# Kernel optimization log

Measured on AMD Instinct MI355X. Metric: run time of the kernel, lower is better.

## Reference

```python
import jax, jax.numpy as jnp
import numpy as np

MAX_REL = 128  # max_relative_position


def setup_inputs() -> dict:
    key = jax.random.key(0)
    k1, k2, k3, k4 = jax.random.split(key, 4)
    B, H, S, D = 2, 8, 2048, 64
    q = jax.random.normal(k1, (B, H, S, D), dtype=jnp.float32)
    k = jax.random.normal(k2, (B, H, S, D), dtype=jnp.float32)
    v = jax.random.normal(k3, (B, H, S, D), dtype=jnp.float32)
    rel_table = jax.random.normal(k4, (2 * MAX_REL + 1, D), dtype=jnp.float32)
    return {"q": q, "k": k, "v": v, "rel_table": rel_table}


def reference(q, k, v, rel_table):
    B, H, S, D = q.shape
    scale = jnp.sqrt(jnp.asarray(D, q.dtype))
    # content scores: [B,H,S,S]
    qk_scores = jnp.einsum('bhqd,bhkd->bhqk', q, k)
    # relative position index matrix [S,S] clamped to [-MAX_REL, MAX_REL]
    pos = jnp.arange(S)
    rel_idx = jnp.clip(pos[None, :] - pos[:, None], -MAX_REL, MAX_REL) + MAX_REL
    rel_emb = rel_table[rel_idx]  # [S,S,D]
    # relative scores: per-query dot with rel embedding row -> [B,H,S,S]
    rel_scores = jnp.einsum('bhqd,qkd->bhqk', q, rel_emb)
    scores = (qk_scores + rel_scores) / scale
    attn = jax.nn.softmax(scores, axis=-1)
    # output: [B,H,S,D]
    return jnp.einsum('bhqk,bhkd->bhqd', attn, v)
```

## Files before the change

kernel.cpp:

```cpp
#include <hip/hip_runtime.h>

typedef _Float16 half8 __attribute__((ext_vector_type(8)));
typedef _Float16 half4 __attribute__((ext_vector_type(4)));
typedef float f32x4 __attribute__((ext_vector_type(4)));

#define S_LEN 2048
#define HDIM 64
#define QBLK 64
#define KVBLK 64
#define NT (S_LEN / KVBLK)
#define QRS 258
#define NBH 16
#define L2E 1.44269504f
#define TSTR 72

__device__ __forceinline__ void load_lds16(const void* g, void* l) {
    __builtin_amdgcn_global_load_lds(
        (const __attribute__((address_space(1))) unsigned int*)g,
        (__attribute__((address_space(3))) unsigned int*)l, 16, 0, 0);
}

__global__ __launch_bounds__(256)
void convert_kv_kernel(const float* __restrict__ Kg, const float* __restrict__ Vg,
                       _Float16* __restrict__ Kh, _Float16* __restrict__ Vp)
{
    __shared__ _Float16 tile[KVBLK * TSTR];
    const int bid = blockIdx.x;
    const int tid = threadIdx.x;
    if (bid < 1024) {
        const int id = bid * 256 + tid;
        const int r  = id >> 3;
        const int d0 = (id & 7) * 8;
        const float* src = Kg + (size_t)r * HDIM + d0;
        f32x4 f0 = *(const f32x4*)(src);
        f32x4 f1 = *(const f32x4*)(src + 4);
        half8 h;
#pragma unroll
        for (int j = 0; j < 4; ++j) { h[j] = (_Float16)f0[j]; h[j+4] = (_Float16)f1[j]; }
        const int bh = r >> 11, kvg = r & 2047;
        const int t = kvg >> 6, kv = kvg & 63;
        const size_t blk = (size_t)(bh * NT + t) * 8192;
        const int off = (kv * 128 + d0 * 2) ^ ((kv & 7) << 4);
        *(half8*)((char*)Kh + blk + off) = h;
    } else {
        const int bt = bid - 1024;
        const int bh = bt >> 5, t = bt & 31;
        {
            const int kv = tid >> 2;
            const int d0 = (tid & 3) * 16;
            const float* src = Vg + ((size_t)bh * S_LEN + t * KVBLK + kv) * HDIM + d0;
            f32x4 f0 = *(const f32x4*)(src);
            f32x4 f1 = *(const f32x4*)(src + 4);
            f32x4 f2 = *(const f32x4*)(src + 8);
            f32x4 f3 = *(const f32x4*)(src + 12);
            half8 h0, h1;
#pragma unroll
            for (int j = 0; j < 4; ++j) {
                h0[j] = (_Float16)f0[j]; h0[j+4] = (_Float16)f1[j];
                h1[j] = (_Float16)f2[j]; h1[j+4] = (_Float16)f3[j];
            }
            *(half8*)&tile[kv * TSTR + d0]     = h0;
            *(half8*)&tile[kv * TSTR + d0 + 8] = h1;
        }
        __syncthreads();
        {
            const int dp = tid >> 2;
            const int u0 = (tid & 3) * 2;
            char* base = (char*)Vp + (size_t)bt * 8192;
            const int swz = (dp & 7) << 4;
#pragma unroll
            for (int ui = 0; ui < 2; ++ui) {
                const int u  = u0 + ui;
                const int kc = u >> 2, g = u & 3;
                half8 ch;
#pragma unroll
                for (int r = 0; r < 4; ++r) {
                    ch[r]     = tile[(32*kc + 4*g + r)      * TSTR + dp];
                    ch[4 + r] = tile[(32*kc + 16 + 4*g + r) * TSTR + dp];
                }
                *(half8*)(base + ((dp * 128 + u * 16) ^ swz)) = ch;
            }
        }
    }
}

__global__ __launch_bounds__(256, 2)
void relattn_v3(const float* __restrict__ Qg, const float* __restrict__ RELg,
                const _Float16* __restrict__ Kh, const _Float16* __restrict__ Vp,
                float* __restrict__ Og)
{
    __shared__ __attribute__((aligned(16))) _Float16 Kbuf[2][4096];
    __shared__ __attribute__((aligned(16))) _Float16 Vbuf[2][4096];
    __shared__ __attribute__((aligned(16))) _Float16 Qrel[QBLK * QRS];

    const int tid  = threadIdx.x;
    const int wave = tid >> 6;
    const int lane = tid & 63;
    const int c = lane & 15;
    const int g = lane >> 4;

    const int wk = ((blockIdx.x & 7) << 6) + (blockIdx.x >> 3);
    const int bh = wk >> 5;
    const int q0 = (wk & 31) * QBLK;

    const size_t hoff = (size_t)bh * S_LEN * HDIM;

    const int qg_ = q0 + wave * 16 + c;
    half8 aq[2];
#pragma unroll
    for (int kc = 0; kc < 2; ++kc) {
        const float* src = Qg + hoff + (size_t)qg_ * HDIM + kc * 32 + g * 8;
        f32x4 f0 = *(const f32x4*)(src);
        f32x4 f1 = *(const f32x4*)(src + 4);
        half8 h;
#pragma unroll
        for (int j = 0; j < 4; ++j) {
            h[j]     = (_Float16)(f0[j] * 0.125f);
            h[j + 4] = (_Float16)(f1[j] * 0.125f);
        }
        aq[kc] = h;
    }

#pragma unroll 1
    for (int t = 0; t < 17; ++t) {
        f32x4 acc = {0.f, 0.f, 0.f, 0.f};
        int r = t * 16 + c;
        if (r > 256) r = 256;
#pragma unroll
        for (int kc = 0; kc < 2; ++kc) {
            const float* src = RELg + (size_t)r * HDIM + kc * 32 + g * 8;
            f32x4 f0 = *(const f32x4*)(src);
            f32x4 f1 = *(const f32x4*)(src + 4);
            half8 b;
#pragma unroll
            for (int j = 0; j < 4; ++j) { b[j] = (_Float16)f0[j]; b[j+4] = (_Float16)f1[j]; }
            acc = __builtin_amdgcn_mfma_f32_16x16x32_f16(aq[kc], b, acc, 0, 0, 0);
        }
        const int col = t * 16 + c;
        if (col <= 256) {
#pragma unroll
            for (int reg = 0; reg < 4; ++reg)
                Qrel[(wave * 16 + 4 * g + reg) * QRS + col] = (_Float16)acc[reg];
        }
    }
    asm volatile("s_waitcnt lgkmcnt(0)" ::: "memory");
    const _Float16* qr = &Qrel[(wave * 16 + c) * QRS];
    const float bias_lo = (float)qr[0];
    const float bias_hi = (float)qr[256];

    const int swz  = (c & 7) << 4;
    const int off0 = (g * 16) ^ swz;
    const int off1 = (64 + g * 16) ^ swz;
    const char* kp0 = (const char*)Kbuf + c * 128 + off0;
    const char* kp1 = (const char*)Kbuf + c * 128 + off1;
    const char* vp0 = (const char*)Vbuf + c * 128 + off0;
    const char* vp1 = (const char*)Vbuf + c * 128 + off1;

    half8 ones;
#pragma unroll
    for (int j = 0; j < 8; ++j) ones[j] = (_Float16)1.0f;

    float m = -1e30f;
    f32x4 l_acc = {0.f, 0.f, 0.f, 0.f};
    f32x4 oacc[4];
#pragma unroll
    for (int i = 0; i < 4; ++i) oacc[i] = (f32x4){0.f, 0.f, 0.f, 0.f};

    const char* kbase = (const char*)Kh + (size_t)(bh * NT) * 8192;
    const char* vbase = (const char*)Vp + (size_t)(bh * NT) * 8192;
    const int goff = wave * 2048 + lane * 16;
    const int loff = wave * 2048;

#define ISSUE(tt, bb) do {                                              \
        const char* kt = kbase + (size_t)(tt) * 8192 + goff;            \
        const char* vt = vbase + (size_t)(tt) * 8192 + goff;            \
        char* kl = (char*)Kbuf + (bb) * 8192 + loff;                    \
        char* vl = (char*)Vbuf + (bb) * 8192 + loff;                    \
        load_lds16(kt,        kl);                                      \
        load_lds16(kt + 1024, kl + 1024);                               \
        load_lds16(vt,        vl);                                      \
        load_lds16(vt + 1024, vl + 1024);                               \
    } while (0)

#define BODY(t, b) do {                                                              \
        if ((t) + 1 < NT) {                                                          \
            ISSUE((t) + 1, (b) ^ 1);                                                 \
            asm volatile("s_waitcnt vmcnt(4)" ::: "memory");                         \
        } else {                                                                     \
            asm volatile("s_waitcnt vmcnt(0)" ::: "memory");                         \
        }                                                                            \
        __builtin_amdgcn_s_barrier();                                                \
        const int k0 = (t) * KVBLK;                                                  \
        f32x4 sacc[4];                                                               \
        _Pragma("unroll")                                                            \
        for (int n = 0; n < 4; ++n) sacc[n] = (f32x4){0.f,0.f,0.f,0.f};              \
        __builtin_amdgcn_s_setprio(1);                                               \
        _Pragma("unroll")                                                            \
        for (int n = 0; n < 4; ++n) {                                                \
            half8 ak0 = *(const half8*)(kp0 + (b) * 8192 + n * 2048);                \
            sacc[n] = __builtin_amdgcn_mfma_f32_16x16x32_f16(ak0, aq[0], sacc[n], 0, 0, 0); \
        }                                                                            \
        _Pragma("unroll")                                                            \
        for (int n = 0; n < 4; ++n) {                                                \
            half8 ak1 = *(const half8*)(kp1 + (b) * 8192 + n * 2048);                \
            sacc[n] = __builtin_amdgcn_mfma_f32_16x16x32_f16(ak1, aq[1], sacc[n], 0, 0, 0); \
        }                                                                            \
        __builtin_amdgcn_s_setprio(0);                                               \
        const bool band = (k0 + 192 > q0) && (k0 < q0 + 192);                        \
        float fold; float mtb;                                                       \
        if (!band) {                                                                 \
            const float bc = (k0 < q0) ? bias_lo : bias_hi;                          \
            float mt = sacc[0][0];                                                   \
            _Pragma("unroll")                                                        \
            for (int n = 0; n < 4; ++n)                                              \
                _Pragma("unroll")                                                    \
                for (int r = 0; r < 4; ++r) mt = fmaxf(mt, sacc[n][r]);              \
            mt = fmaxf(mt, __shfl_xor(mt, 16, 64));                                  \
            mt = fmaxf(mt, __shfl_xor(mt, 32, 64));                                  \
            mtb = mt + bc;                                                           \
            if (!__all(mtb <= m + 8.f)) {                                            \
                const float mnew = fmaxf(m, mtb);                                    \
                const float al = __builtin_amdgcn_exp2f((m - mnew) * L2E);           \
                m = mnew;                                                            \
                _Pragma("unroll")                                                    \
                for (int r = 0; r < 4; ++r) {                                        \
                    const float ar = __shfl(al, 20 * g + r, 64);                     \
                    l_acc[r] *= ar;                                                  \
                    _Pragma("unroll")                                                \
                    for (int dn = 0; dn < 4; ++dn) oacc[dn][r] *= ar;                \
                }                                                                    \
            }                                                                        \
            fold = (bc - m) * L2E;                                                   \
        } else {                                                                     \
            const int base_d = k0 + 4 * g - qg_ + 128;                               \
            float mt = -1e30f;                                                       \
            _Pragma("unroll")                                                        \
            for (int n = 0; n < 4; ++n) {                                            \
                _Pragma("unroll")                                                    \
                for (int r = 0; r < 4; ++r) {                                        \
                    int idx = base_d + 16 * n + r;                                   \
                    idx = idx < 0 ? 0 : (idx > 256 ? 256 : idx);                     \
                    sacc[n][r] += (float)qr[idx];                                    \
                    mt = fmaxf(mt, sacc[n][r]);                                      \
                }                                                                    \
            }                                                                        \
            mt = fmaxf(mt, __shfl_xor(mt, 16, 64));                                  \
            mt = fmaxf(mt, __shfl_xor(mt, 32, 64));                                  \
            mtb = mt;                                                                \
            if (!__all(mtb <= m + 8.f)) {                                            \
                const float mnew = fmaxf(m, mtb);                                    \
                const float al = __builtin_amdgcn_exp2f((m - mnew) * L2E);           \
                m = mnew;                                                            \
                _Pragma("unroll")                                                    \
                for (int r = 0; r < 4; ++r) {                                        \
                    const float ar = __shfl(al, 20 * g + r, 64);                     \
                    l_acc[r] *= ar;                                                  \
                    _Pragma("unroll")                                                \
                    for (int dn = 0; dn < 4; ++dn) oacc[dn][r] *= ar;                \
                }                                                                    \
            }                                                                        \
            fold = -m * L2E;                                                         \
        }                                                                            \
        half4 p4[4];                                                                 \
        _Pragma("unroll")                                                            \
        for (int n = 0; n < 4; ++n) {                                                \
            _Pragma("unroll")                                                        \
            for (int r = 0; r < 4; ++r) {                                            \
                const float pv = __builtin_amdgcn_exp2f(fmaf(sacc[n][r], L2E, fold));\
                p4[n][r] = (_Float16)pv;                                             \
            }                                                                        \
        }                                                                            \
        half8 ap0, ap1;                                                              \
        _Pragma("unroll")                                                            \
        for (int r = 0; r < 4; ++r) {                                                \
            ap0[r] = p4[0][r]; ap0[4 + r] = p4[1][r];                                \
            ap1[r] = p4[2][r]; ap1[4 + r] = p4[3][r];                                \
        }                                                                            \
        __builtin_amdgcn_s_setprio(1);                                               \
        l_acc = __builtin_amdgcn_mfma_f32_16x16x32_f16(ap0, ones, l_acc, 0, 0, 0);   \
        l_acc = __builtin_amdgcn_mfma_f32_16x16x32_f16(ap1, ones, l_acc, 0, 0, 0);   \
        _Pragma("unroll")                                                            \
        for (int dn = 0; dn < 4; ++dn) {                                             \
            half8 bv0 = *(const half8*)(vp0 + (b) * 8192 + dn * 2048);               \
            oacc[dn] = __builtin_amdgcn_mfma_f32_16x16x32_f16(ap0, bv0, oacc[dn], 0, 0, 0); \
        }                                                                            \
        _Pragma("unroll")                                                            \
        for (int dn = 0; dn < 4; ++dn) {                                             \
            half8 bv1 = *(const half8*)(vp1 + (b) * 8192 + dn * 2048);               \
            oacc[dn] = __builtin_amdgcn_mfma_f32_16x16x32_f16(ap1, bv1, oacc[dn], 0, 0, 0); \
        }                                                                            \
        __builtin_amdgcn_s_setprio(0);                                               \
        __builtin_amdgcn_s_barrier();                                                \
    } while (0)

    ISSUE(0, 0);
#pragma unroll 1
    for (int tt = 0; tt < NT; tt += 2) {
        BODY(tt, 0);
        BODY(tt + 1, 1);
    }
#undef BODY
#undef ISSUE

#pragma unroll
    for (int r = 0; r < 4; ++r) {
        const float inv = 1.0f / l_acc[r];
        float* dst = Og + hoff + (size_t)(q0 + wave * 16 + 4 * g + r) * HDIM + c;
#pragma unroll
        for (int dn = 0; dn < 4; ++dn)
            dst[16 * dn] = oacc[dn][r] * inv;
    }
}

__global__ __launch_bounds__(256, 2)
void relattn_v1(const float* __restrict__ Qg, const float* __restrict__ Kg,
                const float* __restrict__ Vg, const float* __restrict__ RELg,
                float* __restrict__ Og)
{
    __shared__ _Float16 Klds[KVBLK * HDIM];
    __shared__ _Float16 Vt[HDIM * KVBLK];
    __shared__ _Float16 Plds[4][16 * KVBLK];
    __shared__ _Float16 Qrel[QBLK * QRS];

    const int tid  = threadIdx.x;
    const int wave = tid >> 6;
    const int lane = tid & 63;
    const int c = lane & 15;
    const int g = lane >> 4;

    const int bid = blockIdx.x;
    const int bh  = bid >> 5;
    const int q0  = (bid & 31) * QBLK;

    const size_t hoff = (size_t)bh * S_LEN * HDIM;
    const float* Qh = Qg + hoff;
    const float* Kh = Kg + hoff;
    const float* Vh = Vg + hoff;

    const int qrow_frag = q0 + wave * 16 + c;
    half8 aq[2];
#pragma unroll
    for (int kc = 0; kc < 2; ++kc) {
        const float* src = Qh + (size_t)qrow_frag * HDIM + kc * 32 + g * 8;
        f32x4 f0 = *(const f32x4*)(src);
        f32x4 f1 = *(const f32x4*)(src + 4);
        half8 h;
#pragma unroll
        for (int j = 0; j < 4; ++j) {
            h[j]     = (_Float16)(f0[j] * 0.125f);
            h[j + 4] = (_Float16)(f1[j] * 0.125f);
        }
        aq[kc] = h;
    }

#pragma unroll 1
    for (int t = 0; t < 17; ++t) {
        f32x4 acc = {0.f, 0.f, 0.f, 0.f};
        int r = t * 16 + c;
        if (r > 256) r = 256;
#pragma unroll
        for (int kc = 0; kc < 2; ++kc) {
            const float* src = RELg + (size_t)r * HDIM + kc * 32 + g * 8;
            f32x4 f0 = *(const f32x4*)(src);
            f32x4 f1 = *(const f32x4*)(src + 4);
            half8 b;
#pragma unroll
            for (int j = 0; j < 4; ++j) { b[j] = (_Float16)f0[j]; b[j+4] = (_Float16)f1[j]; }
            acc = __builtin_amdgcn_mfma_f32_16x16x32_f16(aq[kc], b, acc, 0, 0, 0);
        }
        const int col = t * 16 + c;
        if (col <= 256) {
#pragma unroll
            for (int reg = 0; reg < 4; ++reg)
                Qrel[(wave * 16 + 4 * g + reg) * QRS + col] = (_Float16)acc[reg];
        }
    }

    float mrow[4], lrow[4];
    f32x4 oacc[4];
#pragma unroll
    for (int i = 0; i < 4; ++i) {
        mrow[i] = -1e30f; lrow[i] = 0.f;
        oacc[i] = (f32x4){0.f, 0.f, 0.f, 0.f};
    }

    for (int k0 = 0; k0 < S_LEN; k0 += KVBLK) {
        __syncthreads();
        {
            const int r  = tid >> 2;
            const int dq = (tid & 3) << 4;
            const float* src = Kh + (size_t)(k0 + r) * HDIM + dq;
            f32x4 f0 = *(const f32x4*)(src);
            f32x4 f1 = *(const f32x4*)(src + 4);
            f32x4 f2 = *(const f32x4*)(src + 8);
            f32x4 f3 = *(const f32x4*)(src + 12);
            half8 h0, h1;
#pragma unroll
            for (int j = 0; j < 4; ++j) {
                h0[j] = (_Float16)f0[j]; h0[j+4] = (_Float16)f1[j];
                h1[j] = (_Float16)f2[j]; h1[j+4] = (_Float16)f3[j];
            }
            const int swz = (r & 7) << 4;
            char* base = (char*)Klds;
            *(half8*)(base + ((r * 128 + dq * 2) ^ swz))      = h0;
            *(half8*)(base + ((r * 128 + dq * 2 + 16) ^ swz)) = h1;
        }
        {
            const int kv = tid & 63;
            const int dbase = (tid >> 6) << 4;
            const float* src = Vh + (size_t)(k0 + kv) * HDIM + dbase;
            f32x4 f0 = *(const f32x4*)(src);
            f32x4 f1 = *(const f32x4*)(src + 4);
            f32x4 f2 = *(const f32x4*)(src + 8);
            f32x4 f3 = *(const f32x4*)(src + 12);
            float vals[16];
#pragma unroll
            for (int j = 0; j < 4; ++j) {
                vals[j] = f0[j]; vals[4+j] = f1[j]; vals[8+j] = f2[j]; vals[12+j] = f3[j];
            }
            char* base = (char*)Vt;
#pragma unroll
            for (int i = 0; i < 16; ++i) {
                const int d = dbase + i;
                const int off = (d * 128 + kv * 2) ^ ((d & 7) << 4);
                *(_Float16*)(base + off) = (_Float16)vals[i];
            }
        }
        __syncthreads();

        f32x4 sacc[4];
#pragma unroll
        for (int n = 0; n < 4; ++n) sacc[n] = (f32x4){0.f,0.f,0.f,0.f};
#pragma unroll
        for (int kc = 0; kc < 2; ++kc) {
#pragma unroll
            for (int n = 0; n < 4; ++n) {
                const int off = (((16*n + c) * 128) + kc * 64 + g * 16) ^ ((c & 7) << 4);
                half8 bk = *(const half8*)((const char*)Klds + off);
                sacc[n] = __builtin_amdgcn_mfma_f32_16x16x32_f16(aq[kc], bk, sacc[n], 0, 0, 0);
            }
        }

        float sval[4][4];
        const int myq0 = q0 + wave * 16 + 4 * g;
#pragma unroll
        for (int n = 0; n < 4; ++n) {
            const int kpos = k0 + 16 * n + c;
#pragma unroll
            for (int reg = 0; reg < 4; ++reg) {
                int rel = kpos - (myq0 + reg);
                rel = rel < -128 ? -128 : (rel > 128 ? 128 : rel);
                const float bias = (float)Qrel[(wave*16 + 4*g + reg) * QRS + (rel + 128)];
                sval[n][reg] = sacc[n][reg] + bias;
            }
        }

        float mt[4];
#pragma unroll
        for (int reg = 0; reg < 4; ++reg) {
            float mp = fmaxf(fmaxf(sval[0][reg], sval[1][reg]),
                             fmaxf(sval[2][reg], sval[3][reg]));
#pragma unroll
            for (int msk = 1; msk < 16; msk <<= 1)
                mp = fmaxf(mp, __shfl_xor(mp, msk, 64));
            mt[reg] = mp;
        }

        float alpha[4], psum[4];
#pragma unroll
        for (int reg = 0; reg < 4; ++reg) {
            const float mn = fmaxf(mrow[reg], mt[reg]);
            alpha[reg] = __expf(mrow[reg] - mn);
            mrow[reg] = mn;
            psum[reg] = 0.f;
        }

        char* pbase = (char*)&Plds[wave][0];
#pragma unroll
        for (int n = 0; n < 4; ++n) {
#pragma unroll
            for (int reg = 0; reg < 4; ++reg) {
                const float pv = __expf(sval[n][reg] - mrow[reg]);
                psum[reg] += pv;
                const int row = 4 * g + reg;
                const int off = (row * 128 + (16 * n + c) * 2) ^ ((row & 7) << 4);
                *(_Float16*)(pbase + off) = (_Float16)pv;
            }
        }

#pragma unroll
        for (int reg = 0; reg < 4; ++reg) {
            float ps = psum[reg];
#pragma unroll
            for (int msk = 1; msk < 16; msk <<= 1)
                ps += __shfl_xor(ps, msk, 64);
            lrow[reg] = lrow[reg] * alpha[reg] + ps;
#pragma unroll
            for (int dn = 0; dn < 4; ++dn) oacc[dn][reg] *= alpha[reg];
        }

        asm volatile("s_waitcnt lgkmcnt(0)" ::: "memory");

        half8 ap[2];
#pragma unroll
        for (int kc = 0; kc < 2; ++kc) {
            const int off = (c * 128 + kc * 64 + g * 16) ^ ((c & 7) << 4);
            ap[kc] = *(const half8*)(pbase + off);
        }
#pragma unroll
        for (int kc = 0; kc < 2; ++kc) {
#pragma unroll
            for (int dn = 0; dn < 4; ++dn) {
                const int drow = 16 * dn + c;
                const int off = (drow * 128 + kc * 64 + g * 16) ^ ((c & 7) << 4);
                half8 bv = *(const half8*)((const char*)Vt + off);
                oacc[dn] = __builtin_amdgcn_mfma_f32_16x16x32_f16(ap[kc], bv, oacc[dn], 0, 0, 0);
            }
        }
    }

#pragma unroll
    for (int reg = 0; reg < 4; ++reg) {
        const float inv = 1.0f / lrow[reg];
        const int row = q0 + wave * 16 + 4 * g + reg;
        float* dst = Og + hoff + (size_t)row * HDIM + c;
#pragma unroll
        for (int dn = 0; dn < 4; ++dn)
            dst[16 * dn] = oacc[dn][reg] * inv;
    }
}

extern "C" void kernel_launch(void* const* d_in, const int* in_sizes, int n_in,
                              void* d_out, int out_size, void* d_ws, size_t ws_size,
                              hipStream_t stream) {
    const float* q   = (const float*)d_in[0];
    const float* k   = (const float*)d_in[1];
    const float* v   = (const float*)d_in[2];
    const float* rel = (const float*)d_in[3];
    float* out = (float*)d_out;
    (void)in_sizes; (void)n_in; (void)out_size;

    const size_t kv_bytes = (size_t)NBH * S_LEN * HDIM * sizeof(_Float16);
    if (ws_size >= 2 * kv_bytes) {
        _Float16* KhB = (_Float16*)d_ws;
        _Float16* VpB = (_Float16*)((char*)d_ws + kv_bytes);
        convert_kv_kernel<<<dim3(1536), 256, 0, stream>>>(k, v, KhB, VpB);
        relattn_v3<<<dim3(NBH * (S_LEN / QBLK)), 256, 0, stream>>>(q, rel, KhB, VpB, out);
    } else {
        relattn_v1<<<dim3(NBH * (S_LEN / QBLK)), 256, 0, stream>>>(q, k, v, rel, out);
    }
}
```

Baseline: 63.49 us.

## Split KV range in two per query block with partial-softmax combine kernel

Doubles the grid by splitting each query block's KV sweep into two halves. Each half writes fp16 partial outputs plus per-row max and sum, and a new combine kernel merges them. V tiles are now read straight from global memory into registers with prefetch instead of being staged in LDS, which lowers LDS use so occupancy can rise to 3 blocks per CU. The costs are an extra kernel launch, round trips of the partials through global memory, fp16 rounding of the unnormalised partial outputs, and higher register pressure.

```diff
diff --git a/kernel.cpp b/kernel.cpp
--- a/kernel.cpp
+++ b/kernel.cpp
@@ -9,6 +9,7 @@
 #define QBLK 64
 #define KVBLK 64
 #define NT (S_LEN / KVBLK)
+#define NHALF 16
 #define QRS 258
 #define NBH 16
 #define L2E 1.44269504f
@@ -67,30 +68,29 @@
             const int dp = tid >> 2;
             const int u0 = (tid & 3) * 2;
             char* base = (char*)Vp + (size_t)bt * 8192;
-            const int swz = (dp & 7) << 4;
 #pragma unroll
             for (int ui = 0; ui < 2; ++ui) {
                 const int u  = u0 + ui;
-                const int kc = u >> 2, g = u & 3;
+                const int kc = u >> 2, gg = u & 3;
                 half8 ch;
 #pragma unroll
                 for (int r = 0; r < 4; ++r) {
-                    ch[r]     = tile[(32*kc + 4*g + r)      * TSTR + dp];
-                    ch[4 + r] = tile[(32*kc + 16 + 4*g + r) * TSTR + dp];
+                    ch[r]     = tile[(32*kc + 4*gg + r)      * TSTR + dp];
+                    ch[4 + r] = tile[(32*kc + 16 + 4*gg + r) * TSTR + dp];
                 }
-                *(half8*)(base + ((dp * 128 + u * 16) ^ swz)) = ch;
+                *(half8*)(base + dp * 128 + u * 16) = ch;
             }
         }
     }
 }
 
-__global__ __launch_bounds__(256, 2)
-void relattn_v3(const float* __restrict__ Qg, const float* __restrict__ RELg,
+__global__ __launch_bounds__(256, 3)
+void relattn_v5(const float* __restrict__ Qg, const float* __restrict__ RELg,
                 const _Float16* __restrict__ Kh, const _Float16* __restrict__ Vp,
-                float* __restrict__ Og)
+                _Float16* __restrict__ Opart, float* __restrict__ Mpart,
+                float* __restrict__ Lpart)
 {
     __shared__ __attribute__((aligned(16))) _Float16 Kbuf[2][4096];
-    __shared__ __attribute__((aligned(16))) _Float16 Vbuf[2][4096];
     __shared__ __attribute__((aligned(16))) _Float16 Qrel[QBLK * QRS];
 
     const int tid  = threadIdx.x;
@@ -99,9 +99,12 @@
     const int c = lane & 15;
     const int g = lane >> 4;
 
-    const int wk = ((blockIdx.x & 7) << 6) + (blockIdx.x >> 3);
-    const int bh = wk >> 5;
-    const int q0 = (wk & 31) * QBLK;
+    const int wk = ((blockIdx.x & 7) << 7) + (blockIdx.x >> 3);
+    const int qb = wk >> 1;
+    const int hv = wk & 1;
+    const int bh = qb >> 5;
+    const int q0 = (qb & 31) * QBLK;
+    const int wk_l = qb * 2 + hv;
 
     const size_t hoff = (size_t)bh * S_LEN * HDIM;
 
@@ -148,14 +151,6 @@
     const float bias_lo = (float)qr[0];
     const float bias_hi = (float)qr[256];
 
-    const int swz  = (c & 7) << 4;
-    const int off0 = (g * 16) ^ swz;
-    const int off1 = (64 + g * 16) ^ swz;
-    const char* kp0 = (const char*)Kbuf + c * 128 + off0;
-    const char* kp1 = (const char*)Kbuf + c * 128 + off1;
-    const char* vp0 = (const char*)Vbuf + c * 128 + off0;
-    const char* vp1 = (const char*)Vbuf + c * 128 + off1;
-
     half8 ones;
 #pragma unroll
     for (int j = 0; j < 8; ++j) ones[j] = (_Float16)1.0f;
@@ -166,29 +161,34 @@
 #pragma unroll
     for (int i = 0; i < 4; ++i) oacc[i] = (f32x4){0.f, 0.f, 0.f, 0.f};
 
-    const char* kbase = (const char*)Kh + (size_t)(bh * NT) * 8192;
-    const char* vbase = (const char*)Vp + (size_t)(bh * NT) * 8192;
+    const char* kbase = (const char*)Kh + (size_t)bh * NT * 8192;
+    const int lk = c * 128 + g * 16;
+    const char* vT = (const char*)Vp + (size_t)bh * NT * 8192 + lk;
     const int goff = wave * 2048 + lane * 16;
     const int loff = wave * 2048;
-
-#define ISSUE(tt, bb) do {                                              \
+    const int tstart = hv * NHALF;
+    const int tend   = tstart + NHALF;
+
+#define ISSUE_K(tt, bb) do {                                            \
         const char* kt = kbase + (size_t)(tt) * 8192 + goff;            \
-        const char* vt = vbase + (size_t)(tt) * 8192 + goff;            \
         char* kl = (char*)Kbuf + (bb) * 8192 + loff;                    \
-        char* vl = (char*)Vbuf + (bb) * 8192 + loff;                    \
         load_lds16(kt,        kl);                                      \
         load_lds16(kt + 1024, kl + 1024);                               \
-        load_lds16(vt,        vl);                                      \
-        load_lds16(vt + 1024, vl + 1024);                               \
     } while (0)
 
-#define BODY(t, b) do {                                                              \
-        if ((t) + 1 < NT) {                                                          \
-            ISSUE((t) + 1, (b) ^ 1);                                                 \
-            asm volatile("s_waitcnt vmcnt(4)" ::: "memory");                         \
-        } else {                                                                     \
-            asm volatile("s_waitcnt vmcnt(0)" ::: "memory");                         \
-        }                                                                            \
+#define LOADV(dst, tt) do {                                             \
+        const char* vt_ = vT + (size_t)(tt) * 8192;                     \
+        _Pragma("unroll")                                               \
+        for (int kc = 0; kc < 2; ++kc)                                  \
+            _Pragma("unroll")                                           \
+            for (int dn = 0; dn < 4; ++dn)                              \
+                dst[kc][dn] = *(const half8*)(vt_ + dn * 2048 + kc * 64); \
+    } while (0)
+
+#define BODY(t, b, VC, VN) do {                                                      \
+        const int tn = ((t) + 1 < tend) ? (t) + 1 : (t);                             \
+        ISSUE_K(tn, (b) ^ 1);                                                        \
+        asm volatile("s_waitcnt vmcnt(10)" ::: "memory");                            \
         __builtin_amdgcn_s_barrier();                                                \
         const int k0 = (t) * KVBLK;                                                  \
         f32x4 sacc[4];                                                               \
@@ -197,17 +197,18 @@
         __builtin_amdgcn_s_setprio(1);                                               \
         _Pragma("unroll")                                                            \
         for (int n = 0; n < 4; ++n) {                                                \
-            half8 ak0 = *(const half8*)(kp0 + (b) * 8192 + n * 2048);                \
+            half8 ak0 = *(const half8*)((const char*)Kbuf + (b)*8192 + c*128 + (g*16 ^ ((c&7)<<4)) + n*2048); \
             sacc[n] = __builtin_amdgcn_mfma_f32_16x16x32_f16(ak0, aq[0], sacc[n], 0, 0, 0); \
         }                                                                            \
         _Pragma("unroll")                                                            \
         for (int n = 0; n < 4; ++n) {                                                \
-            half8 ak1 = *(const half8*)(kp1 + (b) * 8192 + n * 2048);                \
+            half8 ak1 = *(const half8*)((const char*)Kbuf + (b)*8192 + c*128 + ((64 + g*16) ^ ((c&7)<<4)) + n*2048); \
             sacc[n] = __builtin_amdgcn_mfma_f32_16x16x32_f16(ak1, aq[1], sacc[n], 0, 0, 0); \
         }                                                                            \
         __builtin_amdgcn_s_setprio(0);                                               \
+        LOADV(VN, tn);                                                               \
         const bool band = (k0 + 192 > q0) && (k0 < q0 + 192);                        \
-        float fold; float mtb;                                                       \
+        float fold, mtb;                                                             \
         if (!band) {                                                                 \
             const float bc = (k0 < q0) ? bias_lo : bias_hi;                          \
             float mt = sacc[0][0];                                                   \
@@ -280,36 +281,75 @@
         l_acc = __builtin_amdgcn_mfma_f32_16x16x32_f16(ap0, ones, l_acc, 0, 0, 0);   \
         l_acc = __builtin_amdgcn_mfma_f32_16x16x32_f16(ap1, ones, l_acc, 0, 0, 0);   \
         _Pragma("unroll")                                                            \
-        for (int dn = 0; dn < 4; ++dn) {                                             \
-            half8 bv0 = *(const half8*)(vp0 + (b) * 8192 + dn * 2048);               \
-            oacc[dn] = __builtin_amdgcn_mfma_f32_16x16x32_f16(ap0, bv0, oacc[dn], 0, 0, 0); \
-        }                                                                            \
+        for (int dn = 0; dn < 4; ++dn)                                               \
+            oacc[dn] = __builtin_amdgcn_mfma_f32_16x16x32_f16(ap0, VC[0][dn], oacc[dn], 0, 0, 0); \
         _Pragma("unroll")                                                            \
-        for (int dn = 0; dn < 4; ++dn) {                                             \
-            half8 bv1 = *(const half8*)(vp1 + (b) * 8192 + dn * 2048);               \
-            oacc[dn] = __builtin_amdgcn_mfma_f32_16x16x32_f16(ap1, bv1, oacc[dn], 0, 0, 0); \
-        }                                                                            \
+        for (int dn = 0; dn < 4; ++dn)                                               \
+            oacc[dn] = __builtin_amdgcn_mfma_f32_16x16x32_f16(ap1, VC[1][dn], oacc[dn], 0, 0, 0); \
         __builtin_amdgcn_s_setprio(0);                                               \
         __builtin_amdgcn_s_barrier();                                                \
     } while (0)
 
-    ISSUE(0, 0);
+    half8 va[2][4], vb[2][4];
+    ISSUE_K(tstart, 0);
+    LOADV(va, tstart);
+
 #pragma unroll 1
-    for (int tt = 0; tt < NT; tt += 2) {
-        BODY(tt, 0);
-        BODY(tt + 1, 1);
-    }
+    for (int i = 0; i < NHALF; i += 2) {
+        BODY(tstart + i,     0, va, vb);
+        BODY(tstart + i + 1, 1, vb, va);
+    }
+    asm volatile("s_waitcnt vmcnt(0)" ::: "memory");
 #undef BODY
-#undef ISSUE
-
-#pragma unroll
-    for (int r = 0; r < 4; ++r) {
-        const float inv = 1.0f / l_acc[r];
-        float* dst = Og + hoff + (size_t)(q0 + wave * 16 + 4 * g + r) * HDIM + c;
-#pragma unroll
-        for (int dn = 0; dn < 4; ++dn)
-            dst[16 * dn] = oacc[dn][r] * inv;
-    }
+#undef LOADV
+#undef ISSUE_K
+
+    {
+        _Float16* od = Opart + (size_t)wk_l * 4096;
+#pragma unroll
+        for (int r = 0; r < 4; ++r) {
+            const int row = wave * 16 + 4 * g + r;
+#pragma unroll
+            for (int dn = 0; dn < 4; ++dn)
+                od[row * 64 + 16 * dn + c] = (_Float16)oacc[dn][r];
+        }
+        if (g == 0)
+            Mpart[(size_t)wk_l * 64 + wave * 16 + c] = m;
+        if (c == 0) {
+#pragma unroll
+            for (int r = 0; r < 4; ++r)
+                Lpart[(size_t)wk_l * 64 + wave * 16 + 4 * g + r] = l_acc[r];
+        }
+    }
+}
+
+__global__ __launch_bounds__(256)
+void combine_kernel(const _Float16* __restrict__ Opart, const float* __restrict__ Mpart,
+                    const float* __restrict__ Lpart, float* __restrict__ Og)
+{
+    const int tid = threadIdx.x;
+    const int row = blockIdx.x * 16 + (tid >> 4);
+    const int col = (tid & 15) * 4;
+    const int qt  = (row >> 6);
+    const int r64 = row & 63;
+    const int p0 = qt * 2, p1 = p0 + 1;
+
+    const float m0 = Mpart[(size_t)p0 * 64 + r64];
+    const float m1 = Mpart[(size_t)p1 * 64 + r64];
+    const float l0 = Lpart[(size_t)p0 * 64 + r64];
+    const float l1 = Lpart[(size_t)p1 * 64 + r64];
+    const float M  = fmaxf(m0, m1);
+    const float w0 = __builtin_amdgcn_exp2f((m0 - M) * L2E);
+    const float w1 = __builtin_amdgcn_exp2f((m1 - M) * L2E);
+    const float inv = 1.0f / (l0 * w0 + l1 * w1);
+
+    const half4 o0 = *(const half4*)(Opart + (size_t)p0 * 4096 + r64 * 64 + col);
+    const half4 o1 = *(const half4*)(Opart + (size_t)p1 * 4096 + r64 * 64 + col);
+    f32x4 out;
+#pragma unroll
+    for (int j = 0; j < 4; ++j)
+        out[j] = ((float)o0[j] * w0 + (float)o1[j] * w1) * inv;
+    *(f32x4*)(Og + (size_t)row * 64 + col) = out;
 }
 
 __global__ __launch_bounds__(256, 2)
@@ -541,11 +581,20 @@
     (void)in_sizes; (void)n_in; (void)out_size;
 
     const size_t kv_bytes = (size_t)NBH * S_LEN * HDIM * sizeof(_Float16);
-    if (ws_size >= 2 * kv_bytes) {
-        _Float16* KhB = (_Float16*)d_ws;
-        _Float16* VpB = (_Float16*)((char*)d_ws + kv_bytes);
+    const size_t op_bytes = (size_t)1024 * 4096 * sizeof(_Float16);
+    const size_t ml_bytes = (size_t)1024 * 64 * sizeof(float);
+    const size_t need = 2 * kv_bytes + op_bytes + 2 * ml_bytes;
+
+    if (ws_size >= need) {
+        char* p = (char*)d_ws;
+        _Float16* KhB  = (_Float16*)p;                 p += kv_bytes;
+        _Float16* VpB  = (_Float16*)p;                 p += kv_bytes;
+        _Float16* OpB  = (_Float16*)p;                 p += op_bytes;
+        float*    MpB  = (float*)p;                    p += ml_bytes;
+        float*    LpB  = (float*)p;
         convert_kv_kernel<<<dim3(1536), 256, 0, stream>>>(k, v, KhB, VpB);
-        relattn_v3<<<dim3(NBH * (S_LEN / QBLK)), 256, 0, stream>>>(q, rel, KhB, VpB, out);
+        relattn_v5<<<dim3(1024), 256, 0, stream>>>(q, rel, KhB, VpB, OpB, MpB, LpB);
+        combine_kernel<<<dim3(2048), 256, 0, stream>>>(OpB, MpB, LpB, out);
     } else {
         relattn_v1<<<dim3(NBH * (S_LEN / QBLK)), 256, 0, stream>>>(q, k, v, rel, out);
     }
```

Measured after the change: 137.1 us. +115.9%, slower.

## Split KV range across waves with per-wave staging and LDS softmax merge

Applied to the files above, without the earlier changes.

Each wave now processes all 64 query rows against a private slice of the KV tiles, so the four waves of a block no longer share K/V tiles. Each wave has its own LDS staging buffer, which removes the per-tile block barriers. Partial outputs, row maxima and row sums are merged across waves through LDS at the end. The V pre-layout is changed to match a 16x16x16 MFMA B-operand format. The cost is four times the accumulator registers, an extra reduction epilogue, and fp16 rounding of the partial outputs.

```diff
diff --git a/kernel.cpp b/kernel.cpp
--- a/kernel.cpp
+++ b/kernel.cpp
@@ -64,37 +64,35 @@
         }
         __syncthreads();
         {
-            const int dp = tid >> 2;
-            const int u0 = (tid & 3) * 2;
-            char* base = (char*)Vp + (size_t)bt * 8192;
-            const int swz = (dp & 7) << 4;
-#pragma unroll
-            for (int ui = 0; ui < 2; ++ui) {
-                const int u  = u0 + ui;
-                const int kc = u >> 2, g = u & 3;
+            const int w = tid >> 6, lane = tid & 63;
+            const int c = lane & 15, g = lane >> 4;
+            char* base = (char*)Vp + (size_t)bt * 8192 + w * 2048;
+#pragma unroll
+            for (int s = 0; s < 2; ++s) {
                 half8 ch;
 #pragma unroll
-                for (int r = 0; r < 4; ++r) {
-                    ch[r]     = tile[(32*kc + 4*g + r)      * TSTR + dp];
-                    ch[4 + r] = tile[(32*kc + 16 + 4*g + r) * TSTR + dp];
+                for (int j = 0; j < 4; ++j) {
+                    ch[j]     = tile[(16*w + 4*g + j) * TSTR + 32*s + c];
+                    ch[4 + j] = tile[(16*w + 4*g + j) * TSTR + 32*s + 16 + c];
                 }
-                *(half8*)(base + ((dp * 128 + u * 16) ^ swz)) = ch;
+                *(half8*)(base + s * 1024 + lane * 16) = ch;
             }
         }
     }
 }
 
 __global__ __launch_bounds__(256, 2)
-void relattn_v3(const float* __restrict__ Qg, const float* __restrict__ RELg,
+void relattn_v6(const float* __restrict__ Qg, const float* __restrict__ RELg,
                 const _Float16* __restrict__ Kh, const _Float16* __restrict__ Vp,
                 float* __restrict__ Og)
 {
-    __shared__ __attribute__((aligned(16))) _Float16 Kbuf[2][4096];
-    __shared__ __attribute__((aligned(16))) _Float16 Vbuf[2][4096];
+    __shared__ __attribute__((aligned(16))) char Stage[4][8192];
     __shared__ __attribute__((aligned(16))) _Float16 Qrel[QBLK * QRS];
+    __shared__ float MLds[4][64];
+    __shared__ float LLds[4][64];
 
     const int tid  = threadIdx.x;
-    const int wave = tid >> 6;
+    const int w    = tid >> 6;
     const int lane = tid & 63;
     const int c = lane & 15;
     const int g = lane >> 4;
@@ -102,23 +100,25 @@
     const int wk = ((blockIdx.x & 7) << 6) + (blockIdx.x >> 3);
     const int bh = wk >> 5;
     const int q0 = (wk & 31) * QBLK;
-
     const size_t hoff = (size_t)bh * S_LEN * HDIM;
 
-    const int qg_ = q0 + wave * 16 + c;
-    half8 aq[2];
-#pragma unroll
-    for (int kc = 0; kc < 2; ++kc) {
-        const float* src = Qg + hoff + (size_t)qg_ * HDIM + kc * 32 + g * 8;
-        f32x4 f0 = *(const f32x4*)(src);
-        f32x4 f1 = *(const f32x4*)(src + 4);
-        half8 h;
-#pragma unroll
-        for (int j = 0; j < 4; ++j) {
-            h[j]     = (_Float16)(f0[j] * 0.125f);
-            h[j + 4] = (_Float16)(f1[j] * 0.125f);
-        }
-        aq[kc] = h;
+    half8 bq[2][4];
+#pragma unroll
+    for (int qn = 0; qn < 4; ++qn) {
+        const int qrow = q0 + 16 * qn + c;
+#pragma unroll
+        for (int kc = 0; kc < 2; ++kc) {
+            const float* src = Qg + hoff + (size_t)qrow * HDIM + kc * 32 + g * 8;
+            f32x4 f0 = *(const f32x4*)(src);
+            f32x4 f1 = *(const f32x4*)(src + 4);
+            half8 h;
+#pragma unroll
+            for (int j = 0; j < 4; ++j) {
+                h[j]     = (_Float16)(f0[j] * 0.125f);
+                h[j + 4] = (_Float16)(f1[j] * 0.125f);
+            }
+            bq[kc][qn] = h;
+        }
     }
 
 #pragma unroll 1
@@ -134,163 +134,148 @@
             half8 b;
 #pragma unroll
             for (int j = 0; j < 4; ++j) { b[j] = (_Float16)f0[j]; b[j+4] = (_Float16)f1[j]; }
-            acc = __builtin_amdgcn_mfma_f32_16x16x32_f16(aq[kc], b, acc, 0, 0, 0);
+            acc = __builtin_amdgcn_mfma_f32_16x16x32_f16(bq[kc][w], b, acc, 0, 0, 0);
         }
         const int col = t * 16 + c;
         if (col <= 256) {
 #pragma unroll
             for (int reg = 0; reg < 4; ++reg)
-                Qrel[(wave * 16 + 4 * g + reg) * QRS + col] = (_Float16)acc[reg];
-        }
-    }
-    asm volatile("s_waitcnt lgkmcnt(0)" ::: "memory");
-    const _Float16* qr = &Qrel[(wave * 16 + c) * QRS];
-    const float bias_lo = (float)qr[0];
-    const float bias_hi = (float)qr[256];
-
-    const int swz  = (c & 7) << 4;
-    const int off0 = (g * 16) ^ swz;
-    const int off1 = (64 + g * 16) ^ swz;
-    const char* kp0 = (const char*)Kbuf + c * 128 + off0;
-    const char* kp1 = (const char*)Kbuf + c * 128 + off1;
-    const char* vp0 = (const char*)Vbuf + c * 128 + off0;
-    const char* vp1 = (const char*)Vbuf + c * 128 + off1;
-
-    half8 ones;
-#pragma unroll
-    for (int j = 0; j < 8; ++j) ones[j] = (_Float16)1.0f;
-
-    float m = -1e30f;
-    f32x4 l_acc = {0.f, 0.f, 0.f, 0.f};
-    f32x4 oacc[4];
-#pragma unroll
-    for (int i = 0; i < 4; ++i) oacc[i] = (f32x4){0.f, 0.f, 0.f, 0.f};
-
-    const char* kbase = (const char*)Kh + (size_t)(bh * NT) * 8192;
-    const char* vbase = (const char*)Vp + (size_t)(bh * NT) * 8192;
-    const int goff = wave * 2048 + lane * 16;
-    const int loff = wave * 2048;
+                Qrel[(16 * w + 4 * g + reg) * QRS + col] = (_Float16)acc[reg];
+        }
+    }
+    __syncthreads();
+
+    const _Float16* qr[4];
+    float bias_lo[4], bias_hi[4];
+#pragma unroll
+    for (int qn = 0; qn < 4; ++qn) {
+        qr[qn] = &Qrel[(16 * qn + c) * QRS];
+        bias_lo[qn] = (float)qr[qn][0];
+        bias_hi[qn] = (float)qr[qn][256];
+    }
+
+    half4 ones4;
+#pragma unroll
+    for (int j = 0; j < 4; ++j) ones4[j] = (_Float16)1.0f;
+
+    float m[4];
+    f32x4 l_acc[4];
+    f32x4 oacc[4][4];
+#pragma unroll
+    for (int qn = 0; qn < 4; ++qn) {
+        m[qn] = -1e30f;
+        l_acc[qn] = (f32x4){0.f, 0.f, 0.f, 0.f};
+#pragma unroll
+        for (int dn = 0; dn < 4; ++dn) oacc[qn][dn] = (f32x4){0.f, 0.f, 0.f, 0.f};
+    }
+
+    const char* kimg = (const char*)Kh + (size_t)bh * NT * 8192;
+    const char* vimg = (const char*)Vp + (size_t)bh * NT * 8192;
+    char* Sw = &Stage[w][0];
+    const int swz = (c & 7) << 4;
 
 #define ISSUE(tt, bb) do {                                              \
-        const char* kt = kbase + (size_t)(tt) * 8192 + goff;            \
-        const char* vt = vbase + (size_t)(tt) * 8192 + goff;            \
-        char* kl = (char*)Kbuf + (bb) * 8192 + loff;                    \
-        char* vl = (char*)Vbuf + (bb) * 8192 + loff;                    \
-        load_lds16(kt,        kl);                                      \
-        load_lds16(kt + 1024, kl + 1024);                               \
-        load_lds16(vt,        vl);                                      \
-        load_lds16(vt + 1024, vl + 1024);                               \
+        const char* kt = kimg + (size_t)(tt) * 8192 + w * 2048 + lane * 16; \
+        const char* vt = vimg + (size_t)(tt) * 8192 + w * 2048 + lane * 16; \
+        char* d_ = Sw + (bb) * 4096 + lane * 16;                        \
+        load_lds16(kt,        d_);                                      \
+        load_lds16(kt + 1024, d_ + 1024);                               \
+        load_lds16(vt,        d_ + 2048);                               \
+        load_lds16(vt + 1024, d_ + 3072);                               \
     } while (0)
 
 #define BODY(t, b) do {                                                              \
-        if ((t) + 1 < NT) {                                                          \
-            ISSUE((t) + 1, (b) ^ 1);                                                 \
-            asm volatile("s_waitcnt vmcnt(4)" ::: "memory");                         \
-        } else {                                                                     \
-            asm volatile("s_waitcnt vmcnt(0)" ::: "memory");                         \
-        }                                                                            \
-        __builtin_amdgcn_s_barrier();                                                \
+        const int tn = ((t) + 1 < NT) ? (t) + 1 : (t);                               \
+        ISSUE(tn, (b) ^ 1);                                                          \
+        asm volatile("s_waitcnt vmcnt(4)" ::: "memory");                             \
+        const char* kb = Sw + (b) * 4096;                                            \
         const int k0 = (t) * KVBLK;                                                  \
+        half8 ak0 = *(const half8*)(kb + ((c * 128 + g * 16) ^ swz));                \
+        half8 ak1 = *(const half8*)(kb + ((c * 128 + 64 + g * 16) ^ swz));           \
+        half8 vv0 = *(const half8*)(kb + 2048 + lane * 16);                          \
+        half8 vv1 = *(const half8*)(kb + 3072 + lane * 16);                          \
         f32x4 sacc[4];                                                               \
         _Pragma("unroll")                                                            \
-        for (int n = 0; n < 4; ++n) sacc[n] = (f32x4){0.f,0.f,0.f,0.f};              \
+        for (int qn = 0; qn < 4; ++qn) sacc[qn] = (f32x4){0.f,0.f,0.f,0.f};          \
         __builtin_amdgcn_s_setprio(1);                                               \
         _Pragma("unroll")                                                            \
-        for (int n = 0; n < 4; ++n) {                                                \
-            half8 ak0 = *(const half8*)(kp0 + (b) * 8192 + n * 2048);                \
-            sacc[n] = __builtin_amdgcn_mfma_f32_16x16x32_f16(ak0, aq[0], sacc[n], 0, 0, 0); \
-        }                                                                            \
+        for (int qn = 0; qn < 4; ++qn)                                               \
+            sacc[qn] = __builtin_amdgcn_mfma_f32_16x16x32_f16(ak0, bq[0][qn], sacc[qn], 0, 0, 0); \
         _Pragma("unroll")                                                            \
-        for (int n = 0; n < 4; ++n) {                                                \
-            half8 ak1 = *(const half8*)(kp1 + (b) * 8192 + n * 2048);                \
-            sacc[n] = __builtin_amdgcn_mfma_f32_16x16x32_f16(ak1, aq[1], sacc[n], 0, 0, 0); \
-        }                                                                            \
+        for (int qn = 0; qn < 4; ++qn)                                               \
+            sacc[qn] = __builtin_amdgcn_mfma_f32_16x16x32_f16(ak1, bq[1][qn], sacc[qn], 0, 0, 0); \
         __builtin_amdgcn_s_setprio(0);                                               \
         const bool band = (k0 + 192 > q0) && (k0 < q0 + 192);                        \
-        float fold; float mtb;                                                       \
+        float bcv[4], mtb[4];                                                        \
         if (!band) {                                                                 \
-            const float bc = (k0 < q0) ? bias_lo : bias_hi;                          \
-            float mt = sacc[0][0];                                                   \
             _Pragma("unroll")                                                        \
-            for (int n = 0; n < 4; ++n)                                              \
+            for (int qn = 0; qn < 4; ++qn) {                                         \
+                bcv[qn] = (k0 < q0) ? bias_lo[qn] : bias_hi[qn];                     \
+                float mt = fmaxf(fmaxf(sacc[qn][0], sacc[qn][1]),                    \
+                                 fmaxf(sacc[qn][2], sacc[qn][3]));                   \
+                mt = fmaxf(mt, __shfl_xor(mt, 16, 64));                              \
+                mt = fmaxf(mt, __shfl_xor(mt, 32, 64));                              \
+                mtb[qn] = mt + bcv[qn];                                              \
+            }                                                                        \
+        } else {                                                                     \
+            _Pragma("unroll")                                                        \
+            for (int qn = 0; qn < 4; ++qn) {                                         \
+                bcv[qn] = 0.f;                                                       \
+                const int base_qn = k0 + 16 * w + 4 * g - (q0 + 16 * qn + c) + 128;  \
+                float mt = -1e30f;                                                   \
                 _Pragma("unroll")                                                    \
-                for (int r = 0; r < 4; ++r) mt = fmaxf(mt, sacc[n][r]);              \
-            mt = fmaxf(mt, __shfl_xor(mt, 16, 64));                                  \
-            mt = fmaxf(mt, __shfl_xor(mt, 32, 64));                                  \
-            mtb = mt + bc;                                                           \
-            if (!__all(mtb <= m + 8.f)) {                                            \
-                const float mnew = fmaxf(m, mtb);                                    \
-                const float al = __builtin_amdgcn_exp2f((m - mnew) * L2E);           \
-                m = mnew;                                                            \
+                for (int r = 0; r < 4; ++r) {                                        \
+                    int idx = base_qn + r;                                           \
+                    idx = idx < 0 ? 0 : (idx > 256 ? 256 : idx);                     \
+                    sacc[qn][r] += (float)qr[qn][idx];                               \
+                    mt = fmaxf(mt, sacc[qn][r]);                                     \
+                }                                                                    \
+                mt = fmaxf(mt, __shfl_xor(mt, 16, 64));                              \
+                mt = fmaxf(mt, __shfl_xor(mt, 32, 64));                              \
+                mtb[qn] = mt;                                                        \
+            }                                                                        \
+        }                                                                            \
+        const bool okd = (mtb[0] <= m[0] + 8.f) && (mtb[1] <= m[1] + 8.f) &&         \
+                         (mtb[2] <= m[2] + 8.f) && (mtb[3] <= m[3] + 8.f);           \
+        if (!__all(okd)) {                                                           \
+            _Pragma("unroll")                                                        \
+            for (int qn = 0; qn < 4; ++qn) {                                         \
+                const float mnew = fmaxf(m[qn], mtb[qn]);                            \
+                const float al = __builtin_amdgcn_exp2f((m[qn] - mnew) * L2E);       \
+                m[qn] = mnew;                                                        \
                 _Pragma("unroll")                                                    \
                 for (int r = 0; r < 4; ++r) {                                        \
                     const float ar = __shfl(al, 20 * g + r, 64);                     \
-                    l_acc[r] *= ar;                                                  \
+                    l_acc[qn][r] *= ar;                                              \
                     _Pragma("unroll")                                                \
-                    for (int dn = 0; dn < 4; ++dn) oacc[dn][r] *= ar;                \
+                    for (int dn = 0; dn < 4; ++dn) oacc[qn][dn][r] *= ar;            \
                 }                                                                    \
             }                                                                        \
-            fold = (bc - m) * L2E;                                                   \
-        } else {                                                                     \
-            const int base_d = k0 + 4 * g - qg_ + 128;                               \
-            float mt = -1e30f;                                                       \
+        }                                                                            \
+        half4 p4h[4];                                                                \
+        _Pragma("unroll")                                                            \
+        for (int qn = 0; qn < 4; ++qn) {                                             \
+            const float fold = (bcv[qn] - m[qn]) * L2E;                              \
             _Pragma("unroll")                                                        \
-            for (int n = 0; n < 4; ++n) {                                            \
-                _Pragma("unroll")                                                    \
-                for (int r = 0; r < 4; ++r) {                                        \
-                    int idx = base_d + 16 * n + r;                                   \
-                    idx = idx < 0 ? 0 : (idx > 256 ? 256 : idx);                     \
-                    sacc[n][r] += (float)qr[idx];                                    \
-                    mt = fmaxf(mt, sacc[n][r]);                                      \
-                }                                                                    \
-            }                                                                        \
-            mt = fmaxf(mt, __shfl_xor(mt, 16, 64));                                  \
-            mt = fmaxf(mt, __shfl_xor(mt, 32, 64));                                  \
-            mtb = mt;                                                                \
-            if (!__all(mtb <= m + 8.f)) {                                            \
-                const float mnew = fmaxf(m, mtb);                                    \
-                const float al = __builtin_amdgcn_exp2f((m - mnew) * L2E);           \
-                m = mnew;                                                            \
-                _Pragma("unroll")                                                    \
-                for (int r = 0; r < 4; ++r) {                                        \
-                    const float ar = __shfl(al, 20 * g + r, 64);                     \
-                    l_acc[r] *= ar;                                                  \
-                    _Pragma("unroll")                                                \
-                    for (int dn = 0; dn < 4; ++dn) oacc[dn][r] *= ar;                \
-                }                                                                    \
-            }                                                                        \
-            fold = -m * L2E;                                                         \
+            for (int r = 0; r < 4; ++r)                                              \
+                p4h[qn][r] = (_Float16)__builtin_amdgcn_exp2f(fmaf(sacc[qn][r], L2E, fold)); \
         }                                                                            \
-        half4 p4[4];                                                                 \
+        half4 vf0, vf1, vf2, vf3;                                                    \
         _Pragma("unroll")                                                            \
-        for (int n = 0; n < 4; ++n) {                                                \
-            _Pragma("unroll")                                                        \
-            for (int r = 0; r < 4; ++r) {                                            \
-                const float pv = __builtin_amdgcn_exp2f(fmaf(sacc[n][r], L2E, fold));\
-                p4[n][r] = (_Float16)pv;                                             \
-            }                                                                        \
-        }                                                                            \
-        half8 ap0, ap1;                                                              \
-        _Pragma("unroll")                                                            \
-        for (int r = 0; r < 4; ++r) {                                                \
-            ap0[r] = p4[0][r]; ap0[4 + r] = p4[1][r];                                \
-            ap1[r] = p4[2][r]; ap1[4 + r] = p4[3][r];                                \
+        for (int j = 0; j < 4; ++j) {                                                \
+            vf0[j] = vv0[j]; vf1[j] = vv0[4 + j];                                    \
+            vf2[j] = vv1[j]; vf3[j] = vv1[4 + j];                                    \
         }                                                                            \
         __builtin_amdgcn_s_setprio(1);                                               \
-        l_acc = __builtin_amdgcn_mfma_f32_16x16x32_f16(ap0, ones, l_acc, 0, 0, 0);   \
-        l_acc = __builtin_amdgcn_mfma_f32_16x16x32_f16(ap1, ones, l_acc, 0, 0, 0);   \
         _Pragma("unroll")                                                            \
-        for (int dn = 0; dn < 4; ++dn) {                                             \
-            half8 bv0 = *(const half8*)(vp0 + (b) * 8192 + dn * 2048);               \
-            oacc[dn] = __builtin_amdgcn_mfma_f32_16x16x32_f16(ap0, bv0, oacc[dn], 0, 0, 0); \
-        }                                                                            \
-        _Pragma("unroll")                                                            \
-        for (int dn = 0; dn < 4; ++dn) {                                             \
-            half8 bv1 = *(const half8*)(vp1 + (b) * 8192 + dn * 2048);               \
-            oacc[dn] = __builtin_amdgcn_mfma_f32_16x16x32_f16(ap1, bv1, oacc[dn], 0, 0, 0); \
+        for (int qn = 0; qn < 4; ++qn) {                                             \
+            l_acc[qn] = __builtin_amdgcn_mfma_f32_16x16x16f16(p4h[qn], ones4, l_acc[qn], 0, 0, 0); \
+            oacc[qn][0] = __builtin_amdgcn_mfma_f32_16x16x16f16(p4h[qn], vf0, oacc[qn][0], 0, 0, 0); \
+            oacc[qn][1] = __builtin_amdgcn_mfma_f32_16x16x16f16(p4h[qn], vf1, oacc[qn][1], 0, 0, 0); \
+            oacc[qn][2] = __builtin_amdgcn_mfma_f32_16x16x16f16(p4h[qn], vf2, oacc[qn][2], 0, 0, 0); \
+            oacc[qn][3] = __builtin_amdgcn_mfma_f32_16x16x16f16(p4h[qn], vf3, oacc[qn][3], 0, 0, 0); \
         }                                                                            \
         __builtin_amdgcn_s_setprio(0);                                               \
-        __builtin_amdgcn_s_barrier();                                                \
     } while (0)
 
     ISSUE(0, 0);
@@ -301,14 +286,71 @@
     }
 #undef BODY
 #undef ISSUE
-
-#pragma unroll
-    for (int r = 0; r < 4; ++r) {
-        const float inv = 1.0f / l_acc[r];
-        float* dst = Og + hoff + (size_t)(q0 + wave * 16 + 4 * g + r) * HDIM + c;
-#pragma unroll
-        for (int dn = 0; dn < 4; ++dn)
-            dst[16 * dn] = oacc[dn][r] * inv;
+    asm volatile("s_waitcnt vmcnt(0) lgkmcnt(0)" ::: "memory");
+
+    {
+        char* Sb = &Stage[0][0];
+#pragma unroll
+        for (int qn = 0; qn < 4; ++qn) {
+#pragma unroll
+            for (int r = 0; r < 4; ++r) {
+                const int row = 16 * qn + 4 * g + r;
+                const int rs = (row & 7) << 4;
+#pragma unroll
+                for (int dn = 0; dn < 4; ++dn) {
+                    const int d = 16 * dn + c;
+                    *(_Float16*)(Sb + w * 8192 + ((row * 128 + d * 2) ^ rs)) = (_Float16)oacc[qn][dn][r];
+                }
+            }
+        }
+        if (g == 0) {
+#pragma unroll
+            for (int qn = 0; qn < 4; ++qn) MLds[w][16 * qn + c] = m[qn];
+        }
+        if (c == 0) {
+#pragma unroll
+            for (int qn = 0; qn < 4; ++qn)
+#pragma unroll
+                for (int r = 0; r < 4; ++r)
+                    LLds[w][16 * qn + 4 * g + r] = l_acc[qn][r];
+        }
+        __syncthreads();
+
+        const int row = 16 * w + c;
+        const int rs = (c & 7) << 4;
+        float mm[4], ll[4];
+#pragma unroll
+        for (int wp = 0; wp < 4; ++wp) { mm[wp] = MLds[wp][row]; ll[wp] = LLds[wp][row]; }
+        const float M = fmaxf(fmaxf(mm[0], mm[1]), fmaxf(mm[2], mm[3]));
+        float wgt[4], den = 0.f;
+#pragma unroll
+        for (int wp = 0; wp < 4; ++wp) {
+            wgt[wp] = __builtin_amdgcn_exp2f((mm[wp] - M) * L2E);
+            den += wgt[wp] * ll[wp];
+        }
+        const float inv = 1.0f / den;
+        float accv[16];
+#pragma unroll
+        for (int e = 0; e < 16; ++e) accv[e] = 0.f;
+#pragma unroll
+        for (int wp = 0; wp < 4; ++wp) {
+            const char* ob = Sb + wp * 8192;
+            half8 a  = *(const half8*)(ob + ((row * 128 + 32 * g) ^ rs));
+            half8 b2 = *(const half8*)(ob + ((row * 128 + 32 * g + 16) ^ rs));
+#pragma unroll
+            for (int e = 0; e < 8; ++e) {
+                accv[e]     += (float)a[e]  * wgt[wp];
+                accv[8 + e] += (float)b2[e] * wgt[wp];
+            }
+        }
+        float* dst = Og + hoff + (size_t)(q0 + row) * HDIM + 16 * g;
+#pragma unroll
+        for (int u = 0; u < 4; ++u) {
+            f32x4 o;
+#pragma unroll
+            for (int j = 0; j < 4; ++j) o[j] = accv[4 * u + j] * inv;
+            *(f32x4*)(dst + 4 * u) = o;
+        }
     }
 }
 
@@ -545,7 +587,7 @@
         _Float16* KhB = (_Float16*)d_ws;
         _Float16* VpB = (_Float16*)((char*)d_ws + kv_bytes);
         convert_kv_kernel<<<dim3(1536), 256, 0, stream>>>(k, v, KhB, VpB);
-        relattn_v3<<<dim3(NBH * (S_LEN / QBLK)), 256, 0, stream>>>(q, rel, KhB, VpB, out);
+        relattn_v6<<<dim3(NBH * (S_LEN / QBLK)), 256, 0, stream>>>(q, rel, KhB, VpB, out);
     } else {
         relattn_v1<<<dim3(NBH * (S_LEN / QBLK)), 256, 0, stream>>>(q, k, v, rel, out);
     }
```

Result: slower. 73.63 us (+16.0%).
